# Performance work log

Measured on AMD Instinct MI355X. Metric: run time of the kernel, lower is better.

The kernel has to match this reference:

```python
import jax, jax.numpy as jnp
import numpy as np

B, S, D = 2, 4096, 768
H = 12
HD = D // H  # 64


def setup_inputs() -> dict:
    key = jax.random.key(0)
    ks = jax.random.split(key, 5)
    scale = 1.0 / np.sqrt(D)
    x = jax.random.normal(ks[0], (B, S, D), dtype=jnp.float32)
    Wq = jax.random.normal(ks[1], (D, D), dtype=jnp.float32) * scale
    Wk = jax.random.normal(ks[2], (D, D), dtype=jnp.float32) * scale
    Wv = jax.random.normal(ks[3], (D, D), dtype=jnp.float32) * scale
    Wo = jax.random.normal(ks[4], (D, D), dtype=jnp.float32) * scale
    zb = jnp.zeros((D,), dtype=jnp.float32)
    return {"x": x, "Wq": Wq, "bq": zb, "Wk": Wk, "bk": zb, "Wv": Wv, "bv": zb, "Wo": Wo, "bo": zb}


def reference(x, Wq, bq, Wk, bk, Wv, bv, Wo, bo):
    b, s, d = x.shape
    # projections: nn.Linear computes x @ W^T + b; here W is stored as [in, out]-style [D, D]
    def proj(W, bias):
        y = jnp.einsum('bsd,ed->bse', x, W) + bias  # matches torch Linear (weight [out,in])
        return y.reshape(b, s, H, HD).transpose(0, 2, 1, 3)  # [B,H,S,HD]
    q = proj(Wq, bq)
    k = proj(Wk, bk)
    v = proj(Wv, bv)
    att = jnp.einsum('bhqd,bhkd->bhqk', q, k) / np.sqrt(HD).astype(np.float32)
    causal = jnp.tril(jnp.ones((s, s), dtype=bool))
    att = jnp.where(causal, att, -jnp.inf)
    att = jax.nn.softmax(att, axis=-1)  # dropout p=0 (eval)
    y = jnp.einsum('bhqk,bhkd->bhqd', att, v)
    y = y.transpose(0, 2, 1, 3).reshape(b, s, d)
    return jnp.einsum('bsd,ed->bse', y, Wo) + bo
```

## Files before the change

kernel.cpp:

```cpp
#include <hip/hip_runtime.h>
#include <hip/hip_bf16.h>

typedef __bf16 bf16;
typedef __attribute__((ext_vector_type(8))) __bf16 bf16x8;
typedef __attribute__((ext_vector_type(4))) __bf16 bf16x4;
typedef __attribute__((ext_vector_type(4))) float f32x4;
typedef __attribute__((ext_vector_type(16))) float f32x16;

#if __has_builtin(__builtin_amdgcn_permlane32_swap)
#define HAVE_PLSWAP 1
typedef __attribute__((ext_vector_type(2))) unsigned uint2v;
#endif

#define MFMA16(a, b, c) __builtin_amdgcn_mfma_f32_16x16x32_bf16((a), (b), (c), 0, 0, 0)
#define MFMA32(a, b, c) __builtin_amdgcn_mfma_f32_32x32x16_bf16((a), (b), (c), 0, 0, 0)

__device__ __forceinline__ void gload_lds16(const bf16* g, bf16* l) {
  __builtin_amdgcn_global_load_lds(
      (const __attribute__((address_space(1))) void*)g,
      (__attribute__((address_space(3))) void*)l, 16, 0, 0);
}

__device__ __forceinline__ unsigned pkbf(float a, float b) {
  union { unsigned u; bf16 h[2]; } w;
  w.h[0] = (bf16)a; w.h[1] = (bf16)b;
  return w.u;
}

__device__ __forceinline__ float mx3(float a, float b, float c) {
  return fmaxf(fmaxf(a, b), c);
}

__global__ void cvt_all(const float* __restrict__ x,
                        const float* __restrict__ wq, const float* __restrict__ wk,
                        const float* __restrict__ wv, const float* __restrict__ wo,
                        bf16* __restrict__ xb, bf16* __restrict__ Wb) {
  constexpr int NX4 = 6291456 / 4;
  constexpr int NW4 = 589824 / 4;
  constexpr int TOT = NX4 + 4 * NW4;
  int stride = gridDim.x * blockDim.x;
  for (int i = blockIdx.x * blockDim.x + threadIdx.x; i < TOT; i += stride) {
    const float4* src;
    bf16x4* dst;
    if (i < NX4) {
      src = reinterpret_cast<const float4*>(x) + i;
      dst = reinterpret_cast<bf16x4*>(xb) + i;
    } else {
      int j = i - NX4;
      int w = j / NW4, r = j - w * NW4;
      const float* sp = (w == 0) ? wq : (w == 1) ? wk : (w == 2) ? wv : wo;
      src = reinterpret_cast<const float4*>(sp) + r;
      dst = reinterpret_cast<bf16x4*>(Wb) + j;
    }
    float4 v = *src;
    bf16x4 o = {(bf16)v.x, (bf16)v.y, (bf16)v.z, (bf16)v.w};
    *dst = o;
  }
}

template <bool OUT_BF16>
__global__ __launch_bounds__(256) void gemm_bt(
    const bf16* __restrict__ A, const bf16* __restrict__ W,
    const float* __restrict__ b0, const float* __restrict__ b1, const float* __restrict__ b2,
    float* __restrict__ Cf, bf16* __restrict__ Cb,
    int M, int N, int K) {
  const int z = blockIdx.z;
  const bf16* Wz = W + (size_t)z * N * K;
  const float* bias = (z == 0) ? b0 : (z == 1 ? b1 : b2);

  __shared__ alignas(16) bf16 As[128 * 64];
  __shared__ alignas(16) bf16 Bs[128 * 64];

  const int tid = threadIdx.x;
  const int wave = tid >> 6, lane = tid & 63;
  const int lr = lane & 15, lg = lane >> 4;
  const int wr = wave >> 1, wc = wave & 1;
  const int m0 = blockIdx.y * 128, n0 = blockIdx.x * 128;

  f32x4 acc[4][4] = {};

  for (int k0 = 0; k0 < K; k0 += 64) {
    __syncthreads();
#pragma unroll
    for (int j = 0; j < 4; ++j) {
      int cb = j * 256 + wave * 64;
      int c = cb + lane;
      int row = c >> 3, x = c & 7;
      int xs = x ^ (row & 7);
      gload_lds16(&A[(size_t)(m0 + row) * K + k0 + xs * 8], &As[cb * 8]);
      gload_lds16(&Wz[(size_t)(n0 + row) * K + k0 + xs * 8], &Bs[cb * 8]);
    }
    __syncthreads();
#pragma unroll
    for (int kk = 0; kk < 2; ++kk) {
      bf16x8 af[4], bfr[4];
#pragma unroll
      for (int m = 0; m < 4; ++m) {
        int row = wr * 64 + m * 16 + lr;
        int ch = (kk * 4 + lg) ^ (row & 7);
        af[m] = *reinterpret_cast<const bf16x8*>(&As[row * 64 + ch * 8]);
      }
#pragma unroll
      for (int n = 0; n < 4; ++n) {
        int row = wc * 64 + n * 16 + lr;
        int ch = (kk * 4 + lg) ^ (row & 7);
        bfr[n] = *reinterpret_cast<const bf16x8*>(&Bs[row * 64 + ch * 8]);
      }
      __builtin_amdgcn_s_setprio(1);
#pragma unroll
      for (int m = 0; m < 4; ++m)
#pragma unroll
        for (int n = 0; n < 4; ++n)
          acc[m][n] = MFMA16(af[m], bfr[n], acc[m][n]);
      __builtin_amdgcn_s_setprio(0);
    }
  }

#pragma unroll
  for (int m = 0; m < 4; ++m) {
#pragma unroll
    for (int n = 0; n < 4; ++n) {
#pragma unroll
      for (int i = 0; i < 4; ++i) {
        int row = m0 + wr * 64 + m * 16 + lg * 4 + i;
        int col = n0 + wc * 64 + n * 16 + lr;
        float v = acc[m][n][i] + bias[col];
        if constexpr (OUT_BF16)
          (Cb + (size_t)z * M * N)[(size_t)row * N + col] = (bf16)v;
        else
          Cf[(size_t)row * N + col] = v;
      }
    }
  }
}

__global__ __launch_bounds__(256, 3) void attn32(
    const bf16* __restrict__ Q, const bf16* __restrict__ K,
    const bf16* __restrict__ V, bf16* __restrict__ Y) {
  constexpr int S = 4096, D = 768;
  const int lin = blockIdx.x;
  const int xcd = lin & 7, idx = lin >> 3;
  const int seg = idx >> 5;
  const int pair = xcd * 3 + seg;
  const int j = idx & 31;
  const int f = (seg == 0) ? j : (seg == 1) ? (31 - j) : ((j + 16) & 31);
  const int h = pair % 12, bb = pair / 12;

  const int tid = threadIdx.x, wave = tid >> 6, lane = tid & 63;
  const int ln = lane & 31, hi = lane >> 5;

  const int qs = (wave < 2) ? (63 - f) : f;
  const int qw0 = qs * 64 + (wave & 1) * 32;
  const int qrow = qw0 + ln;
  const int nt = 64 - f;

  __shared__ alignas(16) bf16 Ks[2][64 * 64];
  __shared__ alignas(16) bf16 Vt[64 * 64];

  const size_t head = (size_t)bb * S * D + (size_t)h * 64;
  const float SC2 = 0.125f * 1.44269504089f;

  union U32x4 { unsigned u[4]; bf16x8 v; };
  U32x4 onesU;
  onesU.u[0] = onesU.u[1] = onesU.u[2] = onesU.u[3] = 0x3F803F80u;
  const bf16x8 onesf = onesU.v;

  bf16x8 qf[4];
  {
    const bf16* qp = Q + head + (size_t)qrow * D;
#pragma unroll
    for (int c = 0; c < 4; ++c) {
      bf16x8 tq = *reinterpret_cast<const bf16x8*>(qp + c * 16 + hi * 8);
#pragma unroll
      for (int e = 0; e < 8; ++e) tq[e] = (bf16)((float)tq[e] * SC2);
      qf[c] = tq;
    }
  }

  int fOff[4];
#pragma unroll
  for (int i = 0; i < 4; ++i)
    fOff[i] = ln * 64 + ((((2 * i + hi) ^ ln) & 7) * 8);

  const bf16* gk[2];
  int ldsK[2];
#pragma unroll
  for (int j2 = 0; j2 < 2; ++j2) {
    int c = j2 * 256 + tid;
    int r = c >> 3, ch = c & 7;
    gk[j2] = K + head + (size_t)r * D + ((ch ^ (r & 7)) & 7) * 8;
    ldsK[j2] = (j2 * 256 + wave * 64) * 8;
  }

  const int k0v = (tid & 31) * 2, d0 = (tid >> 5) * 8;
  const bf16* gv0 = V + head + (size_t)k0v * D + d0;
  const bf16* gv1 = gv0 + D;
  int wOff[8];
#pragma unroll
  for (int e = 0; e < 8; ++e)
    wOff[e] = (d0 + e) * 64 + ((((k0v >> 3) ^ e) & 7) * 8) + (k0v & 7);

  f32x16 accO0 = {}, accO1 = {}, accL = {};
  float mrun = 8.0f;

  auto stageK = [&](int buf) {
#pragma unroll
    for (int j2 = 0; j2 < 2; ++j2) {
      gload_lds16(gk[j2], &Ks[buf][ldsK[j2]]);
      gk[j2] += 64 * D;
    }
  };
  auto loadV = [&](bf16x8* vv) {
    vv[0] = *reinterpret_cast<const bf16x8*>(gv0);
    vv[1] = *reinterpret_cast<const bf16x8*>(gv1);
    gv0 += 64 * D;
    gv1 += 64 * D;
  };
  auto writeV = [&](const bf16x8* vv) {
#pragma unroll
    for (int e = 0; e < 8; ++e) {
      union { unsigned u; bf16 h[2]; } pw;
      pw.h[0] = vv[0][e]; pw.h[1] = vv[1][e];
      *reinterpret_cast<unsigned*>(&Vt[wOff[e]]) = pw.u;
    }
  };

  {
    bf16x8 v0[2];
    loadV(v0);
    stageK(0);
    writeV(v0);
  }
  __syncthreads();

  int cur = 0;
  for (int t = 0; t < nt; ++t) {
    const int kv0 = t * 64;
    const bool more = (t + 1 < nt);
    bf16x8 vnext[2];
    if (more) {
      loadV(vnext);
      stageK(cur ^ 1);
    }

    if (kv0 <= qw0 + 31) {
      f32x16 s0 = {}, s1 = {};
      __builtin_amdgcn_s_setprio(1);
#pragma unroll
      for (int c = 0; c < 4; ++c) {
        bf16x8 kf0 = *reinterpret_cast<const bf16x8*>(&Ks[cur][fOff[c]]);
        bf16x8 kf1 = *reinterpret_cast<const bf16x8*>(&Ks[cur][fOff[c] + 2048]);
        s0 = MFMA32(kf0, qf[c], s0);
        s1 = MFMA32(kf1, qf[c], s1);
      }
      __builtin_amdgcn_s_setprio(0);

      if (kv0 + 63 > qw0) {
#pragma unroll
        for (int r = 0; r < 16; ++r) {
          int kl = (r & 3) + 8 * (r >> 2) + 4 * hi;
          if (kv0 + kl > qrow) s0[r] = -1e30f;
          if (kv0 + 32 + kl > qrow) s1[r] = -1e30f;
        }
      }

      float p[32];
#pragma unroll
      for (int r = 0; r < 16; ++r) {
        p[r] = __builtin_amdgcn_exp2f(s0[r] - mrun);
        p[16 + r] = __builtin_amdgcn_exp2f(s1[r] - mrun);
      }

      float t0 = mx3(s0[0], s0[1], s0[2]);
      float t1 = mx3(s0[3], s0[4], s0[5]);
      float t2 = mx3(s0[6], s0[7], s0[8]);
      float t3 = mx3(s0[9], s0[10], s0[11]);
      float t4 = mx3(s0[12], s0[13], s0[14]);
      float t5 = mx3(s0[15], s1[0], s1[1]);
      float t6 = mx3(s1[2], s1[3], s1[4]);
      float t7 = mx3(s1[5], s1[6], s1[7]);
      float t8 = mx3(s1[8], s1[9], s1[10]);
      float t9 = mx3(s1[11], s1[12], s1[13]);
      float ta = fmaxf(s1[14], s1[15]);
      float u0 = mx3(t0, t1, t2);
      float u1 = mx3(t3, t4, t5);
      float u2 = mx3(t6, t7, t8);
      float u3 = fmaxf(t9, ta);
      float pm = fmaxf(mx3(u0, u1, u2), u3);

      if (!__all(pm - mrun <= 8.0f)) {
        float pm2 = fmaxf(pm, __shfl_xor(pm, 32));
        float mnew = fmaxf(mrun, pm2);
        float alpha = __builtin_amdgcn_exp2f(mrun - mnew);
        mrun = mnew;
        accL[0] *= alpha;
#pragma unroll
        for (int r = 0; r < 16; ++r) {
          accO0[r] *= alpha; accO1[r] *= alpha;
          p[r] *= alpha; p[16 + r] *= alpha;
        }
      }

      __builtin_amdgcn_s_setprio(1);
#pragma unroll
      for (int kg = 0; kg < 2; ++kg) {
        const float* pv = &p[kg * 16];
        unsigned w0 = pkbf(pv[0], pv[1]), w1 = pkbf(pv[2], pv[3]);
        unsigned w2 = pkbf(pv[4], pv[5]), w3 = pkbf(pv[6], pv[7]);
        unsigned w4 = pkbf(pv[8], pv[9]), w5 = pkbf(pv[10], pv[11]);
        unsigned w6 = pkbf(pv[12], pv[13]), w7 = pkbf(pv[14], pv[15]);
        union { unsigned u[4]; bf16x8 v; } fe, fo;
#if HAVE_PLSWAP
        uint2v r02 = __builtin_amdgcn_permlane32_swap(w0, w2, false, false);
        uint2v r13 = __builtin_amdgcn_permlane32_swap(w1, w3, false, false);
        uint2v r46 = __builtin_amdgcn_permlane32_swap(w4, w6, false, false);
        uint2v r57 = __builtin_amdgcn_permlane32_swap(w5, w7, false, false);
        fe.u[0] = r02.x; fe.u[1] = r13.x; fe.u[2] = r02.y; fe.u[3] = r13.y;
        fo.u[0] = r46.x; fo.u[1] = r57.x; fo.u[2] = r46.y; fo.u[3] = r57.y;
#else
        unsigned X0 = hi ? w0 : w2, X1 = hi ? w1 : w3;
        unsigned X2 = hi ? w4 : w6, X3 = hi ? w5 : w7;
        unsigned Y0 = __shfl_xor((int)X0, 32), Y1 = __shfl_xor((int)X1, 32);
        unsigned Y2 = __shfl_xor((int)X2, 32), Y3 = __shfl_xor((int)X3, 32);
        fe.u[0] = hi ? Y0 : w0; fe.u[1] = hi ? Y1 : w1;
        fe.u[2] = hi ? w2 : Y0; fe.u[3] = hi ? w3 : Y1;
        fo.u[0] = hi ? Y2 : w4; fo.u[1] = hi ? Y3 : w5;
        fo.u[2] = hi ? w6 : Y2; fo.u[3] = hi ? w7 : Y3;
#endif
#pragma unroll
        for (int half = 0; half < 2; ++half) {
          int kc = 2 * kg + half;
          bf16x8 pf = half ? fo.v : fe.v;
          bf16x8 vf0 = *reinterpret_cast<const bf16x8*>(&Vt[fOff[kc]]);
          bf16x8 vf1 = *reinterpret_cast<const bf16x8*>(&Vt[fOff[kc] + 2048]);
          accO0 = MFMA32(vf0, pf, accO0);
          accO1 = MFMA32(vf1, pf, accO1);
          accL = MFMA32(onesf, pf, accL);
        }
      }
      __builtin_amdgcn_s_setprio(0);
    }

    if (more) {
      __syncthreads();
      writeV(vnext);
      __syncthreads();
      cur ^= 1;
    }
  }

  float inv = 1.f / accL[0];
  bf16* yp = Y + head + (size_t)qrow * D;
#pragma unroll
  for (int g = 0; g < 4; ++g) {
    bf16x4 o0, o1;
#pragma unroll
    for (int i = 0; i < 4; ++i) {
      o0[i] = (bf16)(accO0[g * 4 + i] * inv);
      o1[i] = (bf16)(accO1[g * 4 + i] * inv);
    }
    *reinterpret_cast<bf16x4*>(yp + 8 * g + 4 * hi) = o0;
    *reinterpret_cast<bf16x4*>(yp + 32 + 8 * g + 4 * hi) = o1;
  }
}

extern "C" void kernel_launch(void* const* d_in, const int* in_sizes, int n_in,
                              void* d_out, int out_size, void* d_ws, size_t ws_size,
                              hipStream_t stream) {
  const float* x  = (const float*)d_in[0];
  const float* Wq = (const float*)d_in[1];
  const float* bq = (const float*)d_in[2];
  const float* Wk = (const float*)d_in[3];
  const float* bk = (const float*)d_in[4];
  const float* Wv = (const float*)d_in[5];
  const float* bv = (const float*)d_in[6];
  const float* Wo = (const float*)d_in[7];
  const float* bo = (const float*)d_in[8];
  float* out = (float*)d_out;

  constexpr int Bx = 2, S = 4096, Dd = 768;
  constexpr int M = Bx * S;
  constexpr size_t XB = (size_t)M * Dd;
  constexpr size_t WB = (size_t)Dd * Dd;

  char* ws = (char*)d_ws;
  bf16* xb = (bf16*)ws;
  bf16* Wb = (bf16*)(ws + 2 * XB);
  bf16* Qb = (bf16*)(ws + 2 * XB + 8 * WB);
  bf16* Kb = Qb + XB;
  bf16* Vb = Kb + XB;
  bf16* Yb = Vb + XB;

  cvt_all<<<2048, 256, 0, stream>>>(x, Wq, Wk, Wv, Wo, xb, Wb);

  gemm_bt<true><<<dim3(6, 64, 3), 256, 0, stream>>>(
      xb, Wb, bq, bk, bv, nullptr, Qb, M, Dd, Dd);

  attn32<<<dim3(768), 256, 0, stream>>>(Qb, Kb, Vb, Yb);

  gemm_bt<false><<<dim3(6, 64, 1), 256, 0, stream>>>(
      Yb, Wb + 3 * WB, bo, bo, bo, out, nullptr, M, Dd, Dd);
}
```

Before: 190.4 us.

## Triple-buffer K and double-buffer V to use one barrier per tile

The attention kernel now keeps three K tiles and two transposed-V tiles in LDS. K is staged two iterations ahead, and V is written into the alternate buffer. Each iteration's pair of __syncthreads is replaced by one barrier that waits with s_waitcnt vmcnt(2), so the newest K prefetch can stay in flight. The goal is less barrier stalling and more overlap of global-to-LDS traffic with MFMA work. The cost is larger LDS use (40KB), which may lower occupancy, and correctness now depends on getting the manual vmcnt accounting right.

```diff
diff --git a/kernel.cpp b/kernel.cpp
--- a/kernel.cpp
+++ b/kernel.cpp
@@ -30,6 +30,13 @@
 __device__ __forceinline__ float mx3(float a, float b, float c) {
   return fmaxf(fmaxf(a, b), c);
 }
+
+#define CBAR(N)                                               \
+  do {                                                        \
+    asm volatile("s_waitcnt vmcnt(" #N ") lgkmcnt(0)" ::: "memory"); \
+    __builtin_amdgcn_s_barrier();                             \
+    __builtin_amdgcn_sched_barrier(0);                        \
+  } while (0)
 
 __global__ void cvt_all(const float* __restrict__ x,
                         const float* __restrict__ wq, const float* __restrict__ wk,
@@ -154,8 +161,8 @@
   const int qrow = qw0 + ln;
   const int nt = 64 - f;
 
-  __shared__ alignas(16) bf16 Ks[2][64 * 64];
-  __shared__ alignas(16) bf16 Vt[64 * 64];
+  __shared__ alignas(16) bf16 Ks[3][64 * 64];
+  __shared__ alignas(16) bf16 Vt[2][64 * 64];
 
   const size_t head = (size_t)bb * S * D + (size_t)h * 64;
   const float SC2 = 0.125f * 1.44269504089f;
@@ -216,12 +223,12 @@
     gv0 += 64 * D;
     gv1 += 64 * D;
   };
-  auto writeV = [&](const bf16x8* vv) {
+  auto writeV = [&](const bf16x8* vv, int buf) {
 #pragma unroll
     for (int e = 0; e < 8; ++e) {
       union { unsigned u; bf16 h[2]; } pw;
       pw.h[0] = vv[0][e]; pw.h[1] = vv[1][e];
-      *reinterpret_cast<unsigned*>(&Vt[wOff[e]]) = pw.u;
+      *reinterpret_cast<unsigned*>(&Vt[buf][wOff[e]]) = pw.u;
     }
   };
 
@@ -229,27 +236,29 @@
     bf16x8 v0[2];
     loadV(v0);
     stageK(0);
-    writeV(v0);
-  }
-  __syncthreads();
-
-  int cur = 0;
+    stageK(1);
+    writeV(v0, 0);
+  }
+  CBAR(2);
+
+  int curV = 0, curK = 0, sK = 2;
   for (int t = 0; t < nt; ++t) {
     const int kv0 = t * 64;
     const bool more = (t + 1 < nt);
     bf16x8 vnext[2];
     if (more) {
       loadV(vnext);
-      stageK(cur ^ 1);
+      if (t + 2 < nt) { stageK(sK); sK = (sK == 2) ? 0 : sK + 1; }
     }
 
     if (kv0 <= qw0 + 31) {
+      const bf16* ksp = &Ks[curK][0];
       f32x16 s0 = {}, s1 = {};
       __builtin_amdgcn_s_setprio(1);
 #pragma unroll
       for (int c = 0; c < 4; ++c) {
-        bf16x8 kf0 = *reinterpret_cast<const bf16x8*>(&Ks[cur][fOff[c]]);
-        bf16x8 kf1 = *reinterpret_cast<const bf16x8*>(&Ks[cur][fOff[c] + 2048]);
+        bf16x8 kf0 = *reinterpret_cast<const bf16x8*>(ksp + fOff[c]);
+        bf16x8 kf1 = *reinterpret_cast<const bf16x8*>(ksp + fOff[c] + 2048);
         s0 = MFMA32(kf0, qf[c], s0);
         s1 = MFMA32(kf1, qf[c], s1);
       }
@@ -301,6 +310,7 @@
         }
       }
 
+      const bf16* vtp = &Vt[curV][0];
       __builtin_amdgcn_s_setprio(1);
 #pragma unroll
       for (int kg = 0; kg < 2; ++kg) {
@@ -331,8 +341,8 @@
         for (int half = 0; half < 2; ++half) {
           int kc = 2 * kg + half;
           bf16x8 pf = half ? fo.v : fe.v;
-          bf16x8 vf0 = *reinterpret_cast<const bf16x8*>(&Vt[fOff[kc]]);
-          bf16x8 vf1 = *reinterpret_cast<const bf16x8*>(&Vt[fOff[kc] + 2048]);
+          bf16x8 vf0 = *reinterpret_cast<const bf16x8*>(vtp + fOff[kc]);
+          bf16x8 vf1 = *reinterpret_cast<const bf16x8*>(vtp + fOff[kc] + 2048);
           accO0 = MFMA32(vf0, pf, accO0);
           accO1 = MFMA32(vf1, pf, accO1);
           accL = MFMA32(onesf, pf, accL);
@@ -342,10 +352,10 @@
     }
 
     if (more) {
-      __syncthreads();
-      writeV(vnext);
-      __syncthreads();
-      cur ^= 1;
+      writeV(vnext, curV ^ 1);
+      CBAR(2);
+      curV ^= 1;
+      curK = (curK == 2) ? 0 : curK + 1;
     }
   }
 
```

Result: no change. 193.3 us (+1.5%).
